# Kernel tuning notes

Hardware: AMD Instinct MI355X
Metric: run time of the kernel (lower is better)

## Reference

```python
import jax, jax.numpy as jnp
import numpy as np

N_SRC, N_DST, N_EDGES = 60000, 50000, 600000
IN_DIM, OUT_DIM = 256, 128


def setup_inputs() -> dict:
    key = jax.random.key(0)
    k1, k2, k3, k4, k5, k6 = jax.random.split(key, 6)
    features = jax.random.normal(k1, (N_SRC, IN_DIM), dtype=jnp.float32)
    t = jax.random.uniform(k2, (N_SRC,), dtype=jnp.float32)
    edge_src = jax.random.randint(k3, (N_EDGES,), 0, N_SRC, dtype=jnp.int32)
    edge_dst = jax.random.randint(k4, (N_EDGES,), 0, N_DST, dtype=jnp.int32)
    # learned params: xavier_normal with relu gain for fc, default for temporal_fc
    gain = float(np.sqrt(2.0))
    std_fc = gain * np.sqrt(2.0 / (IN_DIM + OUT_DIM))
    W_fc = jax.random.normal(k5, (OUT_DIM, IN_DIM), dtype=jnp.float32) * std_fc
    W_t = jax.random.normal(k6, (1, OUT_DIM), dtype=jnp.float32) * (1.0 / np.sqrt(OUT_DIM))
    return {"features": features, "t": t, "edge_src": edge_src,
            "edge_dst": edge_dst, "n_dst": N_DST, "W_fc": W_fc, "W_t": W_t}


def reference(features, t, edge_src, edge_dst, n_dst, W_fc, W_t):
    # z = fc(h), no bias
    z = features @ W_fc.T                      # [n_src, out_dim]
    s = (z @ W_t.T)[:, 0]                      # temporal_fc(z) -> [n_src]
    # edge attention: e = -|t_src - t_dst| (non-differentiable in original)
    e = jax.lax.stop_gradient(-jnp.abs(t[edge_src] - t[edge_dst]))  # [E]
    # mailbox logits: exp(temporal_fc(z_src) * e / 500)
    y = jnp.exp(s[edge_src] * e / 500.0)       # [E]
    # segment softmax over incoming edges of each dst node
    m = jax.ops.segment_max(y, edge_dst, num_segments=n_dst)
    m = jnp.where(jnp.isfinite(m), m, 0.0)     # empty mailboxes
    ex = jnp.exp(y - m[edge_dst])
    denom = jax.ops.segment_sum(ex, edge_dst, num_segments=n_dst)
    alpha = ex / denom[edge_dst]               # [E]
    # weighted neighbor sum
    h = jax.ops.segment_sum(alpha[:, None] * z[edge_src], edge_dst, num_segments=n_dst)
    # residual
    return z[:n_dst] + h
```

## Files before the change

kernel.cpp:

```cpp
#include <hip/hip_runtime.h>
#include <cstdint>

#define TPB 256
#define DSTRIDE 48

typedef __attribute__((ext_vector_type(8))) _Float16 half8;
typedef __attribute__((ext_vector_type(4))) float floatx4;

__global__ __launch_bounds__(256) void convert_w(
    const float* __restrict__ W, _Float16* __restrict__ Wh, int n)
{
    int i = blockIdx.x * 256 + threadIdx.x;
    if (i < n) Wh[i] = (_Float16)W[i];
}

__global__ __launch_bounds__(512, 4) void gemm_mfma(
    const float* __restrict__ A, const _Float16* __restrict__ Wh,
    const float* __restrict__ Wt, _Float16* __restrict__ z16,
    float* __restrict__ s, int M)
{
    __shared__ half8 Wlds[4096];

    const int tid  = threadIdx.x;
    const int lane = tid & 63;
    const int w    = tid >> 6;
    const int m    = lane & 15;
    const int q    = lane >> 4;

#pragma unroll
    for (int it = 0; it < 8; ++it) {
        int pair = w * 8 + it;
        int nt = pair & 7, ks = pair >> 3;
        const _Float16* src = Wh + (size_t)(nt * 16 + m) * 256 + ks * 32 + q * 8;
        Wlds[pair * 64 + lane] = *(const half8*)src;
    }

    const int row_base = blockIdx.x * 128 + w * 16;
    const int arow = min(row_base + m, M - 1);
    const float* ap = A + (size_t)arow * 256 + q * 8;

    float4 abuf[8];
#pragma unroll
    for (int i = 0; i < 4; ++i) {
        abuf[2 * i]     = *(const float4*)(ap + i * 32);
        abuf[2 * i + 1] = *(const float4*)(ap + i * 32 + 4);
    }

    floatx4 acc[8];
#pragma unroll
    for (int nt = 0; nt < 8; ++nt) acc[nt] = (floatx4){0.f, 0.f, 0.f, 0.f};

    __syncthreads();

#pragma unroll
    for (int ks = 0; ks < 8; ++ks) {
        float4 a0 = abuf[(ks & 3) * 2];
        float4 a1 = abuf[(ks & 3) * 2 + 1];
        half8 af;
        af[0] = (_Float16)a0.x; af[1] = (_Float16)a0.y;
        af[2] = (_Float16)a0.z; af[3] = (_Float16)a0.w;
        af[4] = (_Float16)a1.x; af[5] = (_Float16)a1.y;
        af[6] = (_Float16)a1.z; af[7] = (_Float16)a1.w;

        if (ks < 4) {
            abuf[(ks & 3) * 2]     = *(const float4*)(ap + (ks + 4) * 32);
            abuf[(ks & 3) * 2 + 1] = *(const float4*)(ap + (ks + 4) * 32 + 4);
        }

#pragma unroll
        for (int nt = 0; nt < 8; ++nt) {
            half8 bf = Wlds[(ks * 8 + nt) * 64 + lane];
            acc[nt] = __builtin_amdgcn_mfma_f32_16x16x32_f16(
                af, bf, acc[nt], 0, 0, 0);
        }
    }

    float wt[8];
#pragma unroll
    for (int nt = 0; nt < 8; ++nt) wt[nt] = Wt[nt * 16 + m];

    float sp[4] = {0.f, 0.f, 0.f, 0.f};
#pragma unroll
    for (int nt = 0; nt < 8; ++nt)
#pragma unroll
        for (int reg = 0; reg < 4; ++reg)
            sp[reg] += acc[nt][reg] * wt[nt];

#pragma unroll
    for (int reg = 0; reg < 4; ++reg) {
        int row = row_base + q * 4 + reg;
        if (row < M) {
#pragma unroll
            for (int nt = 0; nt < 8; ++nt)
                z16[(size_t)row * 128 + nt * 16 + m] = (_Float16)acc[nt][reg];
        }
    }
#pragma unroll
    for (int off = 1; off <= 8; off <<= 1)
#pragma unroll
        for (int reg = 0; reg < 4; ++reg)
            sp[reg] += __shfl_xor(sp[reg], off, 64);
    if (m == 0) {
#pragma unroll
        for (int reg = 0; reg < 4; ++reg) {
            int row = row_base + q * 4 + reg;
            if (row < M) s[row] = sp[reg];
        }
    }
}

__global__ __launch_bounds__(256) void scatter_pass(
    const int* __restrict__ esrc, const int* __restrict__ edst,
    const float* __restrict__ t, const float* __restrict__ s,
    int* __restrict__ cnt, int2* __restrict__ edata, int E)
{
    int base = (blockIdx.x * TPB + threadIdx.x) * 4;
    if (base >= E) return;

    int si[4], di[4], pos[4];
    if (base + 3 < E) {
        int4 sv = *(const int4*)(esrc + base);
        int4 dv = *(const int4*)(edst + base);
        si[0] = sv.x; si[1] = sv.y; si[2] = sv.z; si[3] = sv.w;
        di[0] = dv.x; di[1] = dv.y; di[2] = dv.z; di[3] = dv.w;
    } else {
#pragma unroll
        for (int i = 0; i < 4; ++i) {
            int e = min(base + i, E - 1);
            si[i] = esrc[e]; di[i] = edst[e];
        }
    }
    int nv = min(4, E - base);

#pragma unroll
    for (int i = 0; i < 4; ++i)
        pos[i] = (i < nv) ? atomicAdd(&cnt[di[i]], 1) : DSTRIDE;

    float exv[4];
#pragma unroll
    for (int i = 0; i < 4; ++i) {
        float ee = -fabsf(t[si[i]] - t[di[i]]);
        float yv = __expf(s[si[i]] * ee * (1.0f / 500.0f));
        exv[i] = __expf(yv);
    }

#pragma unroll
    for (int i = 0; i < 4; ++i) {
        if (i < nv && pos[i] < DSTRIDE)
            edata[(size_t)di[i] * DSTRIDE + pos[i]] =
                make_int2(si[i], __float_as_int(exv[i]));
    }
}

__global__ __launch_bounds__(256) void aggregate(
    const _Float16* __restrict__ z16, const int* __restrict__ cnt,
    const int2* __restrict__ edata, float* __restrict__ out, int Nd)
{
    int d = blockIdx.x * 4 + (threadIdx.x >> 6);
    if (d >= Nd) return;
    int lane = threadIdx.x & 63;
    int g  = lane >> 4;
    int fo = lane & 15;
    int num = cnt[d];
    if (num > DSTRIDE) num = DSTRIDE;
    const int2* row = edata + (size_t)d * DSTRIDE;

    float acc[8];
#pragma unroll
    for (int i = 0; i < 8; ++i) acc[i] = 0.f;
    float dsum = 0.f;

    int j = g;
    for (; j + 4 < num; j += 8) {
        int2 e0 = row[j];
        int2 e1 = row[j + 4];
        float w0 = __int_as_float(e0.y);
        float w1 = __int_as_float(e1.y);
        half8 v0 = ((const half8*)(z16 + (size_t)e0.x * 128))[fo];
        half8 v1 = ((const half8*)(z16 + (size_t)e1.x * 128))[fo];
        dsum += w0 + w1;
#pragma unroll
        for (int i = 0; i < 8; ++i) {
            acc[i] = fmaf(w0, (float)v0[i], acc[i]);
            acc[i] = fmaf(w1, (float)v1[i], acc[i]);
        }
    }
    for (; j < num; j += 4) {
        int2 e0 = row[j];
        float w0 = __int_as_float(e0.y);
        half8 v0 = ((const half8*)(z16 + (size_t)e0.x * 128))[fo];
        dsum += w0;
#pragma unroll
        for (int i = 0; i < 8; ++i)
            acc[i] = fmaf(w0, (float)v0[i], acc[i]);
    }
    dsum += __shfl_xor(dsum, 16, 64);
    dsum += __shfl_xor(dsum, 32, 64);
    float inv = (num > 0) ? 1.0f / dsum : 0.0f;
#pragma unroll
    for (int i = 0; i < 8; ++i) acc[i] *= inv;
#pragma unroll
    for (int i = 0; i < 8; ++i) {
        acc[i] += __shfl_xor(acc[i], 16, 64);
        acc[i] += __shfl_xor(acc[i], 32, 64);
    }
    if (g == 0) {
        half8 zr = ((const half8*)(z16 + (size_t)d * 128))[fo];
        float* op = out + (size_t)d * 128 + fo * 8;
        float4 o0 = make_float4(acc[0] + (float)zr[0], acc[1] + (float)zr[1],
                                acc[2] + (float)zr[2], acc[3] + (float)zr[3]);
        float4 o1 = make_float4(acc[4] + (float)zr[4], acc[5] + (float)zr[5],
                                acc[6] + (float)zr[6], acc[7] + (float)zr[7]);
        *(float4*)op = o0;
        *(float4*)(op + 4) = o1;
    }
}

extern "C" void kernel_launch(void* const* d_in, const int* in_sizes, int n_in,
                              void* d_out, int out_size, void* d_ws, size_t ws_size,
                              hipStream_t stream)
{
    const float* features = (const float*)d_in[0];
    const float* t        = (const float*)d_in[1];
    const int*   esrc     = (const int*)d_in[2];
    const int*   edst     = (const int*)d_in[3];
    const float* Wfc      = (const float*)d_in[5];
    const float* Wt       = (const float*)d_in[6];
    float* out = (float*)d_out;

    const int M  = in_sizes[1];
    const int E  = in_sizes[2];
    const int OD = in_sizes[6];
    const int Nd = out_size / OD;
    const int ID = in_sizes[5] / OD;

    _Float16* z16 = (_Float16*)d_ws;
    float* s   = (float*)(z16 + (size_t)M * 128);
    int*   cnt = (int*)(s + M);
    _Float16* Wh = (_Float16*)(cnt + Nd);
    int2*  edata = (int2*)(Wh + (size_t)OD * ID);

    (void)hipMemsetAsync(cnt, 0, (size_t)Nd * sizeof(int), stream);

    convert_w<<<(OD * ID + 255) / 256, 256, 0, stream>>>(Wfc, Wh, OD * ID);
    gemm_mfma<<<(M + 127) / 128, 512, 0, stream>>>(features, Wh, Wt, z16, s, M);
    scatter_pass<<<(E / 4 + TPB - 1) / TPB, TPB, 0, stream>>>(esrc, edst, t, s,
                                                              cnt, edata, E);
    aggregate<<<(Nd + 3) / 4, 256, 0, stream>>>(z16, cnt, edata, out, Nd);
}
```

Measured before the change: 188.6 us.

## Fuse edge scatter into GEMM launch and defer exp logits to aggregation

Edge bucketing no longer depends on s. It now runs as extra blocks in the same launch as the MFMA GEMM and stores the raw -|dt| instead of the exponentiated weight. The aggregation kernel gathers s[src] and computes both exponentials per edge. It also switches to 8 edges × 8 column-chunks per wave with 16 accumulators. The GEMM now stages W into LDS in two halves to halve shared memory, which should help the fused kernel's occupancy. The aim is to overlap the atomic scatter with the GEMM and remove one kernel boundary, at the cost of an extra s gather and more registers in aggregation.

```diff
diff --git a/kernel.cpp b/kernel.cpp
--- a/kernel.cpp
+++ b/kernel.cpp
@@ -1,7 +1,6 @@
 #include <hip/hip_runtime.h>
 #include <cstdint>
 
-#define TPB 256
 #define DSTRIDE 48
 
 typedef __attribute__((ext_vector_type(8))) _Float16 half8;
@@ -14,28 +13,61 @@
     if (i < n) Wh[i] = (_Float16)W[i];
 }
 
-__global__ __launch_bounds__(512, 4) void gemm_mfma(
+__global__ __launch_bounds__(512, 4) void fused_main(
     const float* __restrict__ A, const _Float16* __restrict__ Wh,
-    const float* __restrict__ Wt, _Float16* __restrict__ z16,
-    float* __restrict__ s, int M)
-{
-    __shared__ half8 Wlds[4096];
-
+    const float* __restrict__ Wt, const int* __restrict__ esrc,
+    const int* __restrict__ edst, const float* __restrict__ t,
+    _Float16* __restrict__ z16, float* __restrict__ s,
+    int* __restrict__ cnt, int2* __restrict__ edata,
+    int M, int E, int SB)
+{
+    __shared__ half8 Wlds[2048];
+
+    if ((int)blockIdx.x < SB) {
+        int base = (blockIdx.x * 512 + threadIdx.x) * 4;
+        if (base >= E) return;
+
+        int si[4], di[4], pos[4];
+        if (base + 3 < E) {
+            int4 sv = *(const int4*)(esrc + base);
+            int4 dv = *(const int4*)(edst + base);
+            si[0] = sv.x; si[1] = sv.y; si[2] = sv.z; si[3] = sv.w;
+            di[0] = dv.x; di[1] = dv.y; di[2] = dv.z; di[3] = dv.w;
+        } else {
+#pragma unroll
+            for (int i = 0; i < 4; ++i) {
+                int e = min(base + i, E - 1);
+                si[i] = esrc[e]; di[i] = edst[e];
+            }
+        }
+        int nv = min(4, E - base);
+
+#pragma unroll
+        for (int i = 0; i < 4; ++i)
+            pos[i] = (i < nv) ? atomicAdd(&cnt[di[i]], 1) : DSTRIDE;
+
+        float ee[4];
+#pragma unroll
+        for (int i = 0; i < 4; ++i)
+            ee[i] = -fabsf(t[si[i]] - t[di[i]]);
+
+#pragma unroll
+        for (int i = 0; i < 4; ++i) {
+            if (i < nv && pos[i] < DSTRIDE)
+                edata[(size_t)di[i] * DSTRIDE + pos[i]] =
+                    make_int2(si[i], __float_as_int(ee[i]));
+        }
+        return;
+    }
+
+    const int tile = blockIdx.x - SB;
     const int tid  = threadIdx.x;
     const int lane = tid & 63;
     const int w    = tid >> 6;
     const int m    = lane & 15;
     const int q    = lane >> 4;
 
-#pragma unroll
-    for (int it = 0; it < 8; ++it) {
-        int pair = w * 8 + it;
-        int nt = pair & 7, ks = pair >> 3;
-        const _Float16* src = Wh + (size_t)(nt * 16 + m) * 256 + ks * 32 + q * 8;
-        Wlds[pair * 64 + lane] = *(const half8*)src;
-    }
-
-    const int row_base = blockIdx.x * 128 + w * 16;
+    const int row_base = tile * 128 + w * 16;
     const int arow = min(row_base + m, M - 1);
     const float* ap = A + (size_t)arow * 256 + q * 8;
 
@@ -50,28 +82,41 @@
 #pragma unroll
     for (int nt = 0; nt < 8; ++nt) acc[nt] = (floatx4){0.f, 0.f, 0.f, 0.f};
 
-    __syncthreads();
-
-#pragma unroll
-    for (int ks = 0; ks < 8; ++ks) {
-        float4 a0 = abuf[(ks & 3) * 2];
-        float4 a1 = abuf[(ks & 3) * 2 + 1];
-        half8 af;
-        af[0] = (_Float16)a0.x; af[1] = (_Float16)a0.y;
-        af[2] = (_Float16)a0.z; af[3] = (_Float16)a0.w;
-        af[4] = (_Float16)a1.x; af[5] = (_Float16)a1.y;
-        af[6] = (_Float16)a1.z; af[7] = (_Float16)a1.w;
-
-        if (ks < 4) {
-            abuf[(ks & 3) * 2]     = *(const float4*)(ap + (ks + 4) * 32);
-            abuf[(ks & 3) * 2 + 1] = *(const float4*)(ap + (ks + 4) * 32 + 4);
-        }
-
-#pragma unroll
-        for (int nt = 0; nt < 8; ++nt) {
-            half8 bf = Wlds[(ks * 8 + nt) * 64 + lane];
-            acc[nt] = __builtin_amdgcn_mfma_f32_16x16x32_f16(
-                af, bf, acc[nt], 0, 0, 0);
+#pragma unroll
+    for (int h = 0; h < 2; ++h) {
+        __syncthreads();
+#pragma unroll
+        for (int it = 0; it < 4; ++it) {
+            int slot = w * 4 + it;
+            int nt = slot & 7, ks = (slot >> 3) + 4 * h;
+            const _Float16* src =
+                Wh + (size_t)(nt * 16 + m) * 256 + ks * 32 + q * 8;
+            Wlds[slot * 64 + lane] = *(const half8*)src;
+        }
+        __syncthreads();
+
+#pragma unroll
+        for (int k4 = 0; k4 < 4; ++k4) {
+            int ks = h * 4 + k4;
+            float4 a0 = abuf[k4 * 2];
+            float4 a1 = abuf[k4 * 2 + 1];
+            half8 af;
+            af[0] = (_Float16)a0.x; af[1] = (_Float16)a0.y;
+            af[2] = (_Float16)a0.z; af[3] = (_Float16)a0.w;
+            af[4] = (_Float16)a1.x; af[5] = (_Float16)a1.y;
+            af[6] = (_Float16)a1.z; af[7] = (_Float16)a1.w;
+
+            if (ks < 4) {
+                abuf[k4 * 2]     = *(const float4*)(ap + (ks + 4) * 32);
+                abuf[k4 * 2 + 1] = *(const float4*)(ap + (ks + 4) * 32 + 4);
+            }
+
+#pragma unroll
+            for (int nt = 0; nt < 8; ++nt) {
+                half8 bf = Wlds[(k4 * 8 + nt) * 64 + lane];
+                acc[nt] = __builtin_amdgcn_mfma_f32_16x16x32_f16(
+                    af, bf, acc[nt], 0, 0, 0);
+            }
         }
     }
 
@@ -109,110 +154,72 @@
     }
 }
 
-__global__ __launch_bounds__(256) void scatter_pass(
-    const int* __restrict__ esrc, const int* __restrict__ edst,
-    const float* __restrict__ t, const float* __restrict__ s,
-    int* __restrict__ cnt, int2* __restrict__ edata, int E)
-{
-    int base = (blockIdx.x * TPB + threadIdx.x) * 4;
-    if (base >= E) return;
-
-    int si[4], di[4], pos[4];
-    if (base + 3 < E) {
-        int4 sv = *(const int4*)(esrc + base);
-        int4 dv = *(const int4*)(edst + base);
-        si[0] = sv.x; si[1] = sv.y; si[2] = sv.z; si[3] = sv.w;
-        di[0] = dv.x; di[1] = dv.y; di[2] = dv.z; di[3] = dv.w;
-    } else {
-#pragma unroll
-        for (int i = 0; i < 4; ++i) {
-            int e = min(base + i, E - 1);
-            si[i] = esrc[e]; di[i] = edst[e];
-        }
-    }
-    int nv = min(4, E - base);
-
-#pragma unroll
-    for (int i = 0; i < 4; ++i)
-        pos[i] = (i < nv) ? atomicAdd(&cnt[di[i]], 1) : DSTRIDE;
-
-    float exv[4];
-#pragma unroll
-    for (int i = 0; i < 4; ++i) {
-        float ee = -fabsf(t[si[i]] - t[di[i]]);
-        float yv = __expf(s[si[i]] * ee * (1.0f / 500.0f));
-        exv[i] = __expf(yv);
-    }
-
-#pragma unroll
-    for (int i = 0; i < 4; ++i) {
-        if (i < nv && pos[i] < DSTRIDE)
-            edata[(size_t)di[i] * DSTRIDE + pos[i]] =
-                make_int2(si[i], __float_as_int(exv[i]));
-    }
-}
-
 __global__ __launch_bounds__(256) void aggregate(
-    const _Float16* __restrict__ z16, const int* __restrict__ cnt,
-    const int2* __restrict__ edata, float* __restrict__ out, int Nd)
+    const _Float16* __restrict__ z16, const float* __restrict__ s,
+    const int* __restrict__ cnt, const int2* __restrict__ edata,
+    float* __restrict__ out, int Nd)
 {
     int d = blockIdx.x * 4 + (threadIdx.x >> 6);
     if (d >= Nd) return;
     int lane = threadIdx.x & 63;
-    int g  = lane >> 4;
-    int fo = lane & 15;
+    int es = lane >> 3;
+    int c  = lane & 7;
     int num = cnt[d];
     if (num > DSTRIDE) num = DSTRIDE;
     const int2* row = edata + (size_t)d * DSTRIDE;
 
-    float acc[8];
-#pragma unroll
-    for (int i = 0; i < 8; ++i) acc[i] = 0.f;
+    float acc[16];
+#pragma unroll
+    for (int i = 0; i < 16; ++i) acc[i] = 0.f;
     float dsum = 0.f;
 
-    int j = g;
-    for (; j + 4 < num; j += 8) {
-        int2 e0 = row[j];
-        int2 e1 = row[j + 4];
-        float w0 = __int_as_float(e0.y);
-        float w1 = __int_as_float(e1.y);
-        half8 v0 = ((const half8*)(z16 + (size_t)e0.x * 128))[fo];
-        half8 v1 = ((const half8*)(z16 + (size_t)e1.x * 128))[fo];
-        dsum += w0 + w1;
-#pragma unroll
-        for (int i = 0; i < 8; ++i) {
-            acc[i] = fmaf(w0, (float)v0[i], acc[i]);
-            acc[i] = fmaf(w1, (float)v1[i], acc[i]);
-        }
-    }
-    for (; j < num; j += 4) {
-        int2 e0 = row[j];
-        float w0 = __int_as_float(e0.y);
-        half8 v0 = ((const half8*)(z16 + (size_t)e0.x * 128))[fo];
-        dsum += w0;
-#pragma unroll
-        for (int i = 0; i < 8; ++i)
-            acc[i] = fmaf(w0, (float)v0[i], acc[i]);
-    }
-    dsum += __shfl_xor(dsum, 16, 64);
-    dsum += __shfl_xor(dsum, 32, 64);
+    for (int j0 = 0; j0 < num; j0 += 8) {
+        int j = j0 + es;
+        if (j < num) {
+            int2 ed = row[j];
+            float ee = __int_as_float(ed.y);
+            float yv = __expf(s[ed.x] * ee * (1.0f / 500.0f));
+            float exv = __expf(yv);
+            const half8* zp = (const half8*)(z16 + (size_t)ed.x * 128 + c * 16);
+            half8 v0 = zp[0];
+            half8 v1 = zp[1];
+            dsum += exv;
+#pragma unroll
+            for (int i = 0; i < 8; ++i) {
+                acc[i]     = fmaf(exv, (float)v0[i], acc[i]);
+                acc[8 + i] = fmaf(exv, (float)v1[i], acc[8 + i]);
+            }
+        }
+    }
+
+#pragma unroll
+    for (int mask = 8; mask <= 32; mask <<= 1) {
+        dsum += __shfl_xor(dsum, mask, 64);
+#pragma unroll
+        for (int i = 0; i < 16; ++i)
+            acc[i] += __shfl_xor(acc[i], mask, 64);
+    }
+
     float inv = (num > 0) ? 1.0f / dsum : 0.0f;
-#pragma unroll
-    for (int i = 0; i < 8; ++i) acc[i] *= inv;
-#pragma unroll
-    for (int i = 0; i < 8; ++i) {
-        acc[i] += __shfl_xor(acc[i], 16, 64);
-        acc[i] += __shfl_xor(acc[i], 32, 64);
-    }
-    if (g == 0) {
-        half8 zr = ((const half8*)(z16 + (size_t)d * 128))[fo];
-        float* op = out + (size_t)d * 128 + fo * 8;
-        float4 o0 = make_float4(acc[0] + (float)zr[0], acc[1] + (float)zr[1],
-                                acc[2] + (float)zr[2], acc[3] + (float)zr[3]);
-        float4 o1 = make_float4(acc[4] + (float)zr[4], acc[5] + (float)zr[5],
-                                acc[6] + (float)zr[6], acc[7] + (float)zr[7]);
-        *(float4*)op = o0;
-        *(float4*)(op + 4) = o1;
+
+    if (lane < 8) {
+        const half8* zr = (const half8*)(z16 + (size_t)d * 128 + lane * 16);
+        half8 r0 = zr[0], r1 = zr[1];
+        float* op = out + (size_t)d * 128 + lane * 16;
+#pragma unroll
+        for (int v = 0; v < 2; ++v) {
+            const half8& rr = v ? r1 : r0;
+#pragma unroll
+            for (int p = 0; p < 2; ++p) {
+                int b = v * 8 + p * 4;
+                float4 o = make_float4(
+                    fmaf(acc[b + 0], inv, (float)rr[p * 4 + 0]),
+                    fmaf(acc[b + 1], inv, (float)rr[p * 4 + 1]),
+                    fmaf(acc[b + 2], inv, (float)rr[p * 4 + 2]),
+                    fmaf(acc[b + 3], inv, (float)rr[p * 4 + 3]));
+                *(float4*)(op + v * 8 + p * 4) = o;
+            }
+        }
     }
 }
 
@@ -243,8 +250,11 @@
     (void)hipMemsetAsync(cnt, 0, (size_t)Nd * sizeof(int), stream);
 
     convert_w<<<(OD * ID + 255) / 256, 256, 0, stream>>>(Wfc, Wh, OD * ID);
-    gemm_mfma<<<(M + 127) / 128, 512, 0, stream>>>(features, Wh, Wt, z16, s, M);
-    scatter_pass<<<(E / 4 + TPB - 1) / TPB, TPB, 0, stream>>>(esrc, edst, t, s,
-                                                              cnt, edata, E);
-    aggregate<<<(Nd + 3) / 4, 256, 0, stream>>>(z16, cnt, edata, out, Nd);
-}
+
+    const int SB = (E + 2047) / 2048;
+    const int GB = (M + 127) / 128;
+    fused_main<<<SB + GB, 512, 0, stream>>>(features, Wh, Wt, esrc, edst, t,
+                                            z16, s, cnt, edata, M, E, SB);
+
+    aggregate<<<(Nd + 3) / 4, 256, 0, stream>>>(z16, s, cnt, edata, out, Nd);
+}
```

After: 188.5 us. Within noise of the previous version (-0.1%).
